# Kernel optimization log

Hardware: AMD Instinct MI355X
Metric: run time of the kernel (lower is better)

## Reference

```python
import jax, jax.numpy as jnp
import numpy as np

E, T, D, DFF = 8, 16384, 512, 2048  # experts, tokens, d_model, d_ff
ROUTE_P = 0.25  # ~ top_k=2 of E=8


def setup_inputs() -> dict:
    key = jax.random.key(0)
    k_x, k_m, k_w1, k_w2 = jax.random.split(key, 4)
    x = jax.random.normal(k_x, (T, D), dtype=jnp.float32)
    mask = jax.random.bernoulli(k_m, ROUTE_P, (E, T))  # bool [E, T]
    W1 = jax.random.normal(k_w1, (E, D, DFF), dtype=jnp.float32) * (1.0 / np.sqrt(D).astype(np.float32))
    b1 = jnp.zeros((E, DFF), dtype=jnp.float32)
    W2 = jax.random.normal(k_w2, (E, DFF, D), dtype=jnp.float32) * (1.0 / np.sqrt(DFF).astype(np.float32))
    b2 = jnp.zeros((E, D), dtype=jnp.float32)
    return {"x": x, "W1": W1, "b1": b1, "W2": W2, "b2": b2, "mask": mask}


def reference(x, W1, b1, W2, b2, mask):
    # vmapped per-expert FFN on shared tokens; mask zeroes non-routed tokens.
    # h: [E, T, DFF]
    h = jax.nn.gelu(jnp.einsum('td,edf->etf', x, W1) + b1[:, None, :])
    # y: [E, T, D]
    y = jnp.einsum('etf,efd->etd', h, W2) + b2[:, None, :]
    return jnp.where(mask[:, :, None], y, jnp.zeros((), dtype=y.dtype))
```

## Files before the change

### kernel.cpp

```cpp
#include <hip/hip_runtime.h>
#include <hip/hip_bf16.h>

#define NE 8
#define TOK 16384
#define ND 512
#define NF 2048
#define HP 4608
#define MT 36

typedef __attribute__((ext_vector_type(8))) short bf16x8;
typedef __attribute__((ext_vector_type(4))) float f32x4;
typedef unsigned short u16;
typedef unsigned long long u64;

__device__ __forceinline__ u16 f2bf(float f) {
  union { float f; unsigned u; } c; c.f = f;
  unsigned u = c.u;
  return (u16)((u + 0x7FFFu + ((u >> 16) & 1u)) >> 16);
}

__device__ __forceinline__ float gelu_fast(float x) {
  float x2 = x * x;
  float zp = x * __builtin_fmaf(0.10294325f, x2, 2.3022084f);
  float u = __builtin_amdgcn_exp2f(zp);
  float r = __builtin_amdgcn_rcpf(u + 1.0f);
  return x * (1.0f - r);
}

__device__ __forceinline__ void gl_lds16(const void* g, void* l) {
  __builtin_amdgcn_global_load_lds(
      (const __attribute__((address_space(1))) unsigned int*)g,
      (__attribute__((address_space(3))) unsigned int*)l, 16, 0, 0);
}

__device__ __forceinline__ int swzr(int row) { return ((row >> 1) & 3) << 4; }

__global__ void transpose_bf16(const float* __restrict__ in, u16* __restrict__ out,
                               int R, int C) {
  __shared__ float tile[32][33];
  int e = blockIdx.z;
  const float* ip = in + (size_t)e * R * C;
  u16* op = out + (size_t)e * R * C;
  int c0 = blockIdx.x * 32, r0 = blockIdx.y * 32;
  int tx = threadIdx.x & 31, ty = threadIdx.x >> 5;
  for (int i = 0; i < 32; i += 8)
    tile[ty + i][tx] = ip[(size_t)(r0 + ty + i) * C + (c0 + tx)];
  __syncthreads();
  for (int i = 0; i < 32; i += 8)
    op[(size_t)(c0 + ty + i) * R + (r0 + tx)] = f2bf(tile[tx][ty + i]);
}

__global__ void x_to_bf16(const float* __restrict__ x, u16* __restrict__ xbf) {
  int i = blockIdx.x * 256 + threadIdx.x;
  float4 v = ((const float4*)x)[i];
  union { u16 s[4]; u64 ll; } o;
  o.s[0] = f2bf(v.x); o.s[1] = f2bf(v.y); o.s[2] = f2bf(v.z); o.s[3] = f2bf(v.w);
  ((u64*)xbf)[i] = o.ll;
}

__global__ void zero_unmasked(const int* __restrict__ mask, float4* __restrict__ out4) {
  int row = blockIdx.x * 2 + (threadIdx.x >> 7);
  if (mask[row]) return;
  out4[(size_t)row * 128 + (threadIdx.x & 127)] = float4{0.f, 0.f, 0.f, 0.f};
}

__global__ void compact_mask(const int* __restrict__ mask, int* __restrict__ idx,
                             int* __restrict__ counts) {
  int e = blockIdx.x;
  __shared__ int wsum[4];
  __shared__ int base;
  if (threadIdx.x == 0) base = 0;
  const int* m = mask + (size_t)e * TOK;
  int lane = threadIdx.x & 63, w = threadIdx.x >> 6;
  for (int c0 = 0; c0 < TOK; c0 += 256) {
    __syncthreads();
    int i = c0 + threadIdx.x;
    int mi = (m[i] != 0);
    unsigned long long b = __ballot(mi);
    if (lane == 0) wsum[w] = __popcll(b);
    __syncthreads();
    int off = base;
    for (int ww = 0; ww < w; ww++) off += wsum[ww];
    off += __popcll(b & ((1ull << lane) - 1ull));
    if (mi) idx[(size_t)e * TOK + off] = i;
    __syncthreads();
    if (threadIdx.x == 0) base += wsum[0] + wsum[1] + wsum[2] + wsum[3];
  }
  __syncthreads();
  if (threadIdx.x == 0) counts[e] = base;
}

__launch_bounds__(256, 4)
__global__ void gemm1(const u16* __restrict__ xbf, const u16* __restrict__ W1t,
                      const float* __restrict__ b1f, const int* __restrict__ idx,
                      const int* __restrict__ counts, u16* __restrict__ h) {
  const int BPE = (NF / 128) * MT;
  int bid = blockIdx.x;
  int e = bid / BPE, r = bid % BPE;
  int f0 = (r / MT) * 128, t0 = (r % MT) * 128;
  int cnt = counts[e];
  if (t0 >= cnt) return;

  __shared__ __align__(16) u16 As[2][4096];
  __shared__ __align__(16) u16 Bs[2][4096];

  int tid = threadIdx.x, lane = tid & 63, w = tid >> 6;
  int wm = w & 1, wn = w >> 1;
  int l15 = lane & 15, l4 = lane >> 4;
  const int* idxe = idx + (size_t)e * TOK;

  int srow = lane >> 2, scolb = (lane & 3) << 4;
  int ar0 = w * 16 + srow, ar1 = 64 + w * 16 + srow;
  int cm1 = cnt - 1;
  int tk0 = idxe[t0 + ar0 <= cm1 ? t0 + ar0 : cm1];
  int tk1 = idxe[t0 + ar1 <= cm1 ? t0 + ar1 : cm1];
  const char* xb = (const char*)xbf;
  const char* w1 = (const char*)W1t;
  size_t asrc0 = ((size_t)e * NF + f0 + ar0) * 1024 + (scolb ^ swzr(ar0));
  size_t asrc1 = ((size_t)e * NF + f0 + ar1) * 1024 + (scolb ^ swzr(ar1));
  size_t bsrc0 = (size_t)tk0 * 1024 + (scolb ^ swzr(ar0));
  size_t bsrc1 = (size_t)tk1 * 1024 + (scolb ^ swzr(ar1));

  int aoff[4], boff[4];
  #pragma unroll
  for (int i = 0; i < 4; i++) {
    int rowa = wm * 64 + i * 16 + l15;
    aoff[i] = rowa * 64 + ((l4 * 16) ^ swzr(rowa));
    int rowb = wn * 64 + i * 16 + l15;
    boff[i] = rowb * 64 + ((l4 * 16) ^ swzr(rowb));
  }

  auto STAGE = [&](int kb, int c) {
    char* ad = (char*)As + c * 8192 + w * 1024 + lane * 16;
    char* bd = (char*)Bs + c * 8192 + w * 1024 + lane * 16;
    gl_lds16(w1 + asrc0 + kb * 64, ad);
    gl_lds16(w1 + asrc1 + kb * 64, ad + 4096);
    gl_lds16(xb + bsrc0 + kb * 64, bd);
    gl_lds16(xb + bsrc1 + kb * 64, bd + 4096);
  };

  f32x4 acc[4][4];
  #pragma unroll
  for (int i = 0; i < 4; i++)
    #pragma unroll
    for (int j = 0; j < 4; j++) acc[i][j] = (f32x4)(0.0f);

  STAGE(0, 0);
  __syncthreads();
  #pragma unroll
  for (int kb = 0; kb < 16; ++kb) {
    int cur = kb & 1;
    if (kb < 15) STAGE(kb + 1, cur ^ 1);
    const char* ab = (const char*)As + cur * 8192;
    const char* bb = (const char*)Bs + cur * 8192;
    bf16x8 a[4], b[4];
    #pragma unroll
    for (int i = 0; i < 4; i++) a[i] = *(const bf16x8*)(ab + aoff[i]);
    #pragma unroll
    for (int j = 0; j < 4; j++) b[j] = *(const bf16x8*)(bb + boff[j]);
    #pragma unroll
    for (int i = 0; i < 4; i++)
      #pragma unroll
      for (int j = 0; j < 4; j++)
        acc[i][j] = __builtin_amdgcn_mfma_f32_16x16x32_bf16(a[i], b[j], acc[i][j], 0, 0, 0);
    __syncthreads();
  }

  #pragma unroll
  for (int i = 0; i < 4; i++) {
    int fb = f0 + wm * 64 + i * 16 + l4 * 4;
    f32x4 bv = *(const f32x4*)(b1f + (size_t)e * NF + fb);
    #pragma unroll
    for (int j = 0; j < 4; j++) {
      int t = t0 + wn * 64 + j * 16 + l15;
      union { u16 s[4]; u64 ll; } pk;
      #pragma unroll
      for (int jj = 0; jj < 4; jj++)
        pk.s[jj] = f2bf(gelu_fast(acc[i][j][jj] + bv[jj]));
      *(u64*)(h + ((size_t)e * HP + t) * NF + fb) = pk.ll;
    }
  }
}

__launch_bounds__(256, 4)
__global__ void gemm2(const u16* __restrict__ h, const u16* __restrict__ W2t,
                      const float* __restrict__ b2f, const int* __restrict__ idx,
                      const int* __restrict__ counts, float* __restrict__ out) {
  const int BPE = (ND / 128) * MT;
  int bid = blockIdx.x;
  int e = bid / BPE, r = bid % BPE;
  int d0 = (r / MT) * 128, t0 = (r % MT) * 128;
  int cnt = counts[e];
  if (t0 >= cnt) return;

  __shared__ __align__(16) u16 As[2][4096];
  __shared__ __align__(16) u16 Bs[2][4096];

  int tid = threadIdx.x, lane = tid & 63, w = tid >> 6;
  int wm = w & 1, wn = w >> 1;
  int l15 = lane & 15, l4 = lane >> 4;
  const int* idxe = idx + (size_t)e * TOK;

  int srow = lane >> 2, scolb = (lane & 3) << 4;
  int ar0 = w * 16 + srow, ar1 = 64 + w * 16 + srow;
  const char* hb = (const char*)h;
  const char* w2 = (const char*)W2t;
  size_t asrc0 = ((size_t)e * ND + d0 + ar0) * 4096 + (scolb ^ swzr(ar0));
  size_t asrc1 = ((size_t)e * ND + d0 + ar1) * 4096 + (scolb ^ swzr(ar1));
  size_t bsrc0 = ((size_t)e * HP + t0 + ar0) * 4096 + (scolb ^ swzr(ar0));
  size_t bsrc1 = ((size_t)e * HP + t0 + ar1) * 4096 + (scolb ^ swzr(ar1));

  int aoff[4], boff[4];
  #pragma unroll
  for (int i = 0; i < 4; i++) {
    int rowa = wm * 64 + i * 16 + l15;
    aoff[i] = rowa * 64 + ((l4 * 16) ^ swzr(rowa));
    int rowb = wn * 64 + i * 16 + l15;
    boff[i] = rowb * 64 + ((l4 * 16) ^ swzr(rowb));
  }

  auto STAGE = [&](int kb, int c) {
    char* ad = (char*)As + c * 8192 + w * 1024 + lane * 16;
    char* bd = (char*)Bs + c * 8192 + w * 1024 + lane * 16;
    gl_lds16(w2 + asrc0 + kb * 64, ad);
    gl_lds16(w2 + asrc1 + kb * 64, ad + 4096);
    gl_lds16(hb + bsrc0 + kb * 64, bd);
    gl_lds16(hb + bsrc1 + kb * 64, bd + 4096);
  };

  f32x4 acc[4][4];
  #pragma unroll
  for (int i = 0; i < 4; i++)
    #pragma unroll
    for (int j = 0; j < 4; j++) acc[i][j] = (f32x4)(0.0f);

  STAGE(0, 0);
  __syncthreads();
  #pragma unroll 2
  for (int kb = 0; kb < 64; ++kb) {
    int cur = kb & 1;
    if (kb < 63) STAGE(kb + 1, cur ^ 1);
    const char* ab = (const char*)As + cur * 8192;
    const char* bb = (const char*)Bs + cur * 8192;
    bf16x8 a[4], b[4];
    #pragma unroll
    for (int i = 0; i < 4; i++) a[i] = *(const bf16x8*)(ab + aoff[i]);
    #pragma unroll
    for (int j = 0; j < 4; j++) b[j] = *(const bf16x8*)(bb + boff[j]);
    #pragma unroll
    for (int i = 0; i < 4; i++)
      #pragma unroll
      for (int j = 0; j < 4; j++)
        acc[i][j] = __builtin_amdgcn_mfma_f32_16x16x32_bf16(a[i], b[j], acc[i][j], 0, 0, 0);
    __syncthreads();
  }

  #pragma unroll
  for (int i = 0; i < 4; i++) {
    int db = d0 + wm * 64 + i * 16 + l4 * 4;
    f32x4 b2v = *(const f32x4*)(b2f + (size_t)e * ND + db);
    #pragma unroll
    for (int j = 0; j < 4; j++) {
      int t = t0 + wn * 64 + j * 16 + l15;
      if (t < cnt) {
        int tok = idxe[t];
        f32x4 v;
        #pragma unroll
        for (int jj = 0; jj < 4; jj++) v[jj] = acc[i][j][jj] + b2v[jj];
        *(f32x4*)(out + ((size_t)e * TOK + tok) * ND + db) = v;
      }
    }
  }
}

extern "C" void kernel_launch(void* const* d_in, const int* in_sizes, int n_in,
                              void* d_out, int out_size, void* d_ws, size_t ws_size,
                              hipStream_t stream) {
  const float* x  = (const float*)d_in[0];
  const float* W1 = (const float*)d_in[1];
  const float* b1 = (const float*)d_in[2];
  const float* W2 = (const float*)d_in[3];
  const float* b2 = (const float*)d_in[4];
  const int* mask = (const int*)d_in[5];

  char* ws = (char*)d_ws;
  int* counts = (int*)ws;
  int* idx    = (int*)(ws + 1024);
  u16* W1t    = (u16*)(ws + 1024 + (size_t)NE * TOK * 4);
  u16* W2t    = W1t + (size_t)NE * NF * ND;
  u16* xbf    = W2t + (size_t)NE * ND * NF;
  u16* h      = xbf + (size_t)TOK * ND;

  zero_unmasked<<<dim3(NE * TOK / 2), dim3(256), 0, stream>>>(mask, (float4*)d_out);
  transpose_bf16<<<dim3(NF / 32, ND / 32, NE), dim3(256), 0, stream>>>(W1, W1t, ND, NF);
  transpose_bf16<<<dim3(ND / 32, NF / 32, NE), dim3(256), 0, stream>>>(W2, W2t, NF, ND);
  x_to_bf16<<<dim3(TOK * ND / 4 / 256), dim3(256), 0, stream>>>(x, xbf);
  compact_mask<<<dim3(NE), dim3(256), 0, stream>>>(mask, idx, counts);

  gemm1<<<dim3(NE * (NF / 128) * MT), dim3(256), 0, stream>>>(xbf, W1t, b1, idx, counts, h);
  gemm2<<<dim3(NE * (ND / 128) * MT), dim3(256), 0, stream>>>(h, W2t, b2, idx, counts,
                                                              (float*)d_out);
}
```

Measured before the change: 382.4 us.

## Triple-buffer LDS staging with vmcnt waits and a single barrier per k-step

Both GEMM kernels move from double-buffered to triple-buffered LDS tiles. Loads are issued two k-steps ahead, and explicit s_waitcnt vmcnt waits replace the trailing __syncthreads, so each iteration has one barrier. The aim is to hide global-to-LDS load latency behind MFMA work. In exchange, LDS use per block rises from 32KB to 48KB and launch bounds drop to 3 blocks per CU, which lowers occupancy.

Result: no change. 385.8 us (+0.9%).

```diff
diff --git a/kernel.cpp b/kernel.cpp
--- a/kernel.cpp
+++ b/kernel.cpp
@@ -12,6 +12,8 @@
 typedef __attribute__((ext_vector_type(4))) float f32x4;
 typedef unsigned short u16;
 typedef unsigned long long u64;
+
+#define WAITV(n) asm volatile("s_waitcnt vmcnt(" #n ")" ::: "memory")
 
 __device__ __forceinline__ u16 f2bf(float f) {
   union { float f; unsigned u; } c; c.f = f;
@@ -90,7 +92,7 @@
   if (threadIdx.x == 0) counts[e] = base;
 }
 
-__launch_bounds__(256, 4)
+__launch_bounds__(256, 3)
 __global__ void gemm1(const u16* __restrict__ xbf, const u16* __restrict__ W1t,
                       const float* __restrict__ b1f, const int* __restrict__ idx,
                       const int* __restrict__ counts, u16* __restrict__ h) {
@@ -101,8 +103,8 @@
   int cnt = counts[e];
   if (t0 >= cnt) return;
 
-  __shared__ __align__(16) u16 As[2][4096];
-  __shared__ __align__(16) u16 Bs[2][4096];
+  __shared__ __align__(16) u16 As[3][4096];
+  __shared__ __align__(16) u16 Bs[3][4096];
 
   int tid = threadIdx.x, lane = tid & 63, w = tid >> 6;
   int wm = w & 1, wn = w >> 1;
@@ -130,9 +132,9 @@
     boff[i] = rowb * 64 + ((l4 * 16) ^ swzr(rowb));
   }
 
-  auto STAGE = [&](int kb, int c) {
-    char* ad = (char*)As + c * 8192 + w * 1024 + lane * 16;
-    char* bd = (char*)Bs + c * 8192 + w * 1024 + lane * 16;
+  auto STAGE = [&](int kb, int s) {
+    char* ad = (char*)As + s * 8192 + w * 1024 + lane * 16;
+    char* bd = (char*)Bs + s * 8192 + w * 1024 + lane * 16;
     gl_lds16(w1 + asrc0 + kb * 64, ad);
     gl_lds16(w1 + asrc1 + kb * 64, ad + 4096);
     gl_lds16(xb + bsrc0 + kb * 64, bd);
@@ -146,13 +148,17 @@
     for (int j = 0; j < 4; j++) acc[i][j] = (f32x4)(0.0f);
 
   STAGE(0, 0);
-  __syncthreads();
+  STAGE(1, 1);
+
   #pragma unroll
   for (int kb = 0; kb < 16; ++kb) {
-    int cur = kb & 1;
-    if (kb < 15) STAGE(kb + 1, cur ^ 1);
-    const char* ab = (const char*)As + cur * 8192;
-    const char* bb = (const char*)Bs + cur * 8192;
+    int s = kb % 3;
+    if (kb < 15) WAITV(4);
+    else         WAITV(0);
+    __builtin_amdgcn_s_barrier();
+    if (kb < 14) STAGE(kb + 2, (kb + 2) % 3);
+    const char* ab = (const char*)As + s * 8192;
+    const char* bb = (const char*)Bs + s * 8192;
     bf16x8 a[4], b[4];
     #pragma unroll
     for (int i = 0; i < 4; i++) a[i] = *(const bf16x8*)(ab + aoff[i]);
@@ -163,7 +169,6 @@
       #pragma unroll
       for (int j = 0; j < 4; j++)
         acc[i][j] = __builtin_amdgcn_mfma_f32_16x16x32_bf16(a[i], b[j], acc[i][j], 0, 0, 0);
-    __syncthreads();
   }
 
   #pragma unroll
@@ -182,7 +187,7 @@
   }
 }
 
-__launch_bounds__(256, 4)
+__launch_bounds__(256, 3)
 __global__ void gemm2(const u16* __restrict__ h, const u16* __restrict__ W2t,
                       const float* __restrict__ b2f, const int* __restrict__ idx,
                       const int* __restrict__ counts, float* __restrict__ out) {
@@ -193,8 +198,8 @@
   int cnt = counts[e];
   if (t0 >= cnt) return;
 
-  __shared__ __align__(16) u16 As[2][4096];
-  __shared__ __align__(16) u16 Bs[2][4096];
+  __shared__ __align__(16) u16 As[3][4096];
+  __shared__ __align__(16) u16 Bs[3][4096];
 
   int tid = threadIdx.x, lane = tid & 63, w = tid >> 6;
   int wm = w & 1, wn = w >> 1;
@@ -219,9 +224,9 @@
     boff[i] = rowb * 64 + ((l4 * 16) ^ swzr(rowb));
   }
 
-  auto STAGE = [&](int kb, int c) {
-    char* ad = (char*)As + c * 8192 + w * 1024 + lane * 16;
-    char* bd = (char*)Bs + c * 8192 + w * 1024 + lane * 16;
+  auto STAGE = [&](int kb, int s) {
+    char* ad = (char*)As + s * 8192 + w * 1024 + lane * 16;
+    char* bd = (char*)Bs + s * 8192 + w * 1024 + lane * 16;
     gl_lds16(w2 + asrc0 + kb * 64, ad);
     gl_lds16(w2 + asrc1 + kb * 64, ad + 4096);
     gl_lds16(hb + bsrc0 + kb * 64, bd);
@@ -235,13 +240,16 @@
     for (int j = 0; j < 4; j++) acc[i][j] = (f32x4)(0.0f);
 
   STAGE(0, 0);
-  __syncthreads();
-  #pragma unroll 2
-  for (int kb = 0; kb < 64; ++kb) {
-    int cur = kb & 1;
-    if (kb < 63) STAGE(kb + 1, cur ^ 1);
-    const char* ab = (const char*)As + cur * 8192;
-    const char* bb = (const char*)Bs + cur * 8192;
+  STAGE(1, 1);
+
+  int s0 = 0, s1 = 1, s2 = 2;
+  #pragma unroll 3
+  for (int kb = 0; kb < 63; ++kb) {
+    WAITV(4);
+    __builtin_amdgcn_s_barrier();
+    if (kb < 62) STAGE(kb + 2, s2);
+    const char* ab = (const char*)As + s0 * 8192;
+    const char* bb = (const char*)Bs + s0 * 8192;
     bf16x8 a[4], b[4];
     #pragma unroll
     for (int i = 0; i < 4; i++) a[i] = *(const bf16x8*)(ab + aoff[i]);
@@ -252,7 +260,23 @@
       #pragma unroll
       for (int j = 0; j < 4; j++)
         acc[i][j] = __builtin_amdgcn_mfma_f32_16x16x32_bf16(a[i], b[j], acc[i][j], 0, 0, 0);
-    __syncthreads();
+    int tt = s0; s0 = s1; s1 = s2; s2 = tt;
+  }
+  {
+    WAITV(0);
+    __builtin_amdgcn_s_barrier();
+    const char* ab = (const char*)As + s0 * 8192;
+    const char* bb = (const char*)Bs + s0 * 8192;
+    bf16x8 a[4], b[4];
+    #pragma unroll
+    for (int i = 0; i < 4; i++) a[i] = *(const bf16x8*)(ab + aoff[i]);
+    #pragma unroll
+    for (int j = 0; j < 4; j++) b[j] = *(const bf16x8*)(bb + boff[j]);
+    #pragma unroll
+    for (int i = 0; i < 4; i++)
+      #pragma unroll
+      for (int j = 0; j < 4; j++)
+        acc[i][j] = __builtin_amdgcn_mfma_f32_16x16x32_bf16(a[i], b[j], acc[i][j], 0, 0, 0);
   }
 
   #pragma unroll
```

## Restructure MoE GEMMs into 512-thread 128x256 tiles with triple-buffered interleaved pipeline

Applied to the files above, without the earlier changes.

Both expert GEMMs move to 512-thread blocks, each computing a 128x256 output tile with a K step of 64. Staging uses three LDS buffers, so loads run two K-tiles ahead, and a new XOR swizzle matches the wider rows. The K-tile is split into four MFMA phases interleaved with LDS fragment loads and staged global loads, with explicit vmcnt/lgkmcnt waits, barriers and s_setprio around MFMA bursts. This is meant to hide global and LDS latency and raise data reuse per block. In exchange it uses more LDS and registers, which lowers occupancy, and adds more barriers per K-tile.

Result: no change. 380.8 us (-0.4%).

```diff
diff --git a/kernel.cpp b/kernel.cpp
--- a/kernel.cpp
+++ b/kernel.cpp
@@ -6,12 +6,16 @@
 #define ND 512
 #define NF 2048
 #define HP 4608
-#define MT 36
 
 typedef __attribute__((ext_vector_type(8))) short bf16x8;
 typedef __attribute__((ext_vector_type(4))) float f32x4;
 typedef unsigned short u16;
 typedef unsigned long long u64;
+
+#define WAITV(n) asm volatile("s_waitcnt vmcnt(" #n ")" ::: "memory")
+#define LGKM0()  asm volatile("s_waitcnt lgkmcnt(0)" ::: "memory")
+#define SBAR()   __builtin_amdgcn_s_barrier()
+#define PRIO(p)  __builtin_amdgcn_s_setprio(p)
 
 __device__ __forceinline__ u16 f2bf(float f) {
   union { float f; unsigned u; } c; c.f = f;
@@ -32,8 +36,6 @@
       (const __attribute__((address_space(1))) unsigned int*)g,
       (__attribute__((address_space(3))) unsigned int*)l, 16, 0, 0);
 }
-
-__device__ __forceinline__ int swzr(int row) { return ((row >> 1) & 3) << 4; }
 
 __global__ void transpose_bf16(const float* __restrict__ in, u16* __restrict__ out,
                                int R, int C) {
@@ -90,54 +92,73 @@
   if (threadIdx.x == 0) counts[e] = base;
 }
 
-__launch_bounds__(256, 4)
+
+__launch_bounds__(512, 2)
 __global__ void gemm1(const u16* __restrict__ xbf, const u16* __restrict__ W1t,
                       const float* __restrict__ b1f, const int* __restrict__ idx,
                       const int* __restrict__ counts, u16* __restrict__ h) {
-  const int BPE = (NF / 128) * MT;
   int bid = blockIdx.x;
-  int e = bid / BPE, r = bid % BPE;
-  int f0 = (r / MT) * 128, t0 = (r % MT) * 128;
+  int e = bid / 288, r = bid % 288;
+  int f0 = (r / 18) * 128, t0 = (r % 18) * 256;
   int cnt = counts[e];
   if (t0 >= cnt) return;
 
-  __shared__ __align__(16) u16 As[2][4096];
-  __shared__ __align__(16) u16 Bs[2][4096];
+  __shared__ __align__(16) u16 lds[3 * 24576];
 
   int tid = threadIdx.x, lane = tid & 63, w = tid >> 6;
   int wm = w & 1, wn = w >> 1;
   int l15 = lane & 15, l4 = lane >> 4;
   const int* idxe = idx + (size_t)e * TOK;
-
-  int srow = lane >> 2, scolb = (lane & 3) << 4;
-  int ar0 = w * 16 + srow, ar1 = 64 + w * 16 + srow;
   int cm1 = cnt - 1;
-  int tk0 = idxe[t0 + ar0 <= cm1 ? t0 + ar0 : cm1];
-  int tk1 = idxe[t0 + ar1 <= cm1 ? t0 + ar1 : cm1];
+
+  int srow = w * 16 + (lane >> 3);
+  int ssw = ((lane & 7) * 16) ^ ((srow & 7) << 4);
+  const char* w1 = (const char*)W1t;
   const char* xb = (const char*)xbf;
-  const char* w1 = (const char*)W1t;
-  size_t asrc0 = ((size_t)e * NF + f0 + ar0) * 1024 + (scolb ^ swzr(ar0));
-  size_t asrc1 = ((size_t)e * NF + f0 + ar1) * 1024 + (scolb ^ swzr(ar1));
-  size_t bsrc0 = (size_t)tk0 * 1024 + (scolb ^ swzr(ar0));
-  size_t bsrc1 = (size_t)tk1 * 1024 + (scolb ^ swzr(ar1));
-
-  int aoff[4], boff[4];
+  size_t aS = ((size_t)e * NF + f0 + srow) * 1024 + ssw;
+  int tA0 = idxe[(t0 + srow)       <= cm1 ? (t0 + srow)       : cm1];
+  int tA1 = idxe[(t0 + srow + 8)   <= cm1 ? (t0 + srow + 8)   : cm1];
+  int tB0 = idxe[(t0 + srow + 128) <= cm1 ? (t0 + srow + 128) : cm1];
+  int tB1 = idxe[(t0 + srow + 136) <= cm1 ? (t0 + srow + 136) : cm1];
+  size_t xS0 = (size_t)tA0 * 1024 + ssw, xS1 = (size_t)tA1 * 1024 + ssw;
+  size_t xS2 = (size_t)tB0 * 1024 + ssw, xS3 = (size_t)tB1 * 1024 + ssw;
+
+  int aoff[4][2], boff[4][2];
   #pragma unroll
   for (int i = 0; i < 4; i++) {
-    int rowa = wm * 64 + i * 16 + l15;
-    aoff[i] = rowa * 64 + ((l4 * 16) ^ swzr(rowa));
-    int rowb = wn * 64 + i * 16 + l15;
-    boff[i] = rowb * 64 + ((l4 * 16) ^ swzr(rowb));
-  }
-
-  auto STAGE = [&](int kb, int c) {
-    char* ad = (char*)As + c * 8192 + w * 1024 + lane * 16;
-    char* bd = (char*)Bs + c * 8192 + w * 1024 + lane * 16;
-    gl_lds16(w1 + asrc0 + kb * 64, ad);
-    gl_lds16(w1 + asrc1 + kb * 64, ad + 4096);
-    gl_lds16(xb + bsrc0 + kb * 64, bd);
-    gl_lds16(xb + bsrc1 + kb * 64, bd + 4096);
-  };
+    int ra = wm * 64 + i * 16 + l15;
+    int rb = wn * 64 + i * 16 + l15;
+    #pragma unroll
+    for (int ks = 0; ks < 2; ks++) {
+      aoff[i][ks] = ra * 128 + ((ks * 64 + l4 * 16) ^ ((ra & 7) << 4));
+      boff[i][ks] = 16384 + rb * 128 + ((ks * 64 + l4 * 16) ^ ((rb & 7) << 4));
+    }
+  }
+
+  auto SA = [&](int kt, char* bp) {
+    char* d = bp + w * 2048;
+    gl_lds16(w1 + aS + kt * 128, d);
+    gl_lds16(w1 + aS + 8192 + kt * 128, d + 1024);
+  };
+  auto SB0 = [&](int kt, char* bp) {
+    char* d = bp + 16384 + w * 2048;
+    gl_lds16(xb + xS0 + kt * 128, d);
+    gl_lds16(xb + xS1 + kt * 128, d + 1024);
+  };
+  auto SB1 = [&](int kt, char* bp) {
+    char* d = bp + 32768 + w * 2048;
+    gl_lds16(xb + xS2 + kt * 128, d);
+    gl_lds16(xb + xS3 + kt * 128, d + 1024);
+  };
+
+  char* bc = (char*)lds;
+  char* bn = (char*)lds + 49152;
+  char* bs = (char*)lds + 98304;
+
+  SA(0, bc); SB0(0, bc); SB1(0, bc);
+  SA(1, bn); SB0(1, bn); SB1(1, bn);
+  WAITV(6);
+  SBAR();
 
   f32x4 acc[4][4];
   #pragma unroll
@@ -145,25 +166,67 @@
     #pragma unroll
     for (int j = 0; j < 4; j++) acc[i][j] = (f32x4)(0.0f);
 
-  STAGE(0, 0);
-  __syncthreads();
-  #pragma unroll
-  for (int kb = 0; kb < 16; ++kb) {
-    int cur = kb & 1;
-    if (kb < 15) STAGE(kb + 1, cur ^ 1);
-    const char* ab = (const char*)As + cur * 8192;
-    const char* bb = (const char*)Bs + cur * 8192;
-    bf16x8 a[4], b[4];
-    #pragma unroll
-    for (int i = 0; i < 4; i++) a[i] = *(const bf16x8*)(ab + aoff[i]);
-    #pragma unroll
-    for (int j = 0; j < 4; j++) b[j] = *(const bf16x8*)(bb + boff[j]);
-    #pragma unroll
-    for (int i = 0; i < 4; i++)
+  bf16x8 A0[4], A1[4], Ba[2], Bb[2];
+  #pragma unroll
+  for (int i = 0; i < 4; i++) A0[i] = *(const bf16x8*)(bc + aoff[i][0]);
+  Ba[0] = *(const bf16x8*)(bc + boff[0][0]);
+  Ba[1] = *(const bf16x8*)(bc + boff[1][0]);
+
+  const int nt = 8;
+  for (int t = 0; t < nt; ++t) {
+    bool stg = (t + 2 < nt);
+    if (stg) SA(t + 2, bs);
+    Bb[0] = *(const bf16x8*)(bc + boff[2][0]);
+    Bb[1] = *(const bf16x8*)(bc + boff[3][0]);
+    PRIO(1);
+    #pragma unroll
+    for (int i = 0; i < 4; i++) {
+      acc[i][0] = __builtin_amdgcn_mfma_f32_16x16x32_bf16(A0[i], Ba[0], acc[i][0], 0, 0, 0);
+      acc[i][1] = __builtin_amdgcn_mfma_f32_16x16x32_bf16(A0[i], Ba[1], acc[i][1], 0, 0, 0);
+    }
+    PRIO(0);
+    LGKM0(); SBAR();
+    if (stg) SB0(t + 2, bs);
+    #pragma unroll
+    for (int i = 0; i < 4; i++) A1[i] = *(const bf16x8*)(bc + aoff[i][1]);
+    Ba[0] = *(const bf16x8*)(bc + boff[0][1]);
+    Ba[1] = *(const bf16x8*)(bc + boff[1][1]);
+    PRIO(1);
+    #pragma unroll
+    for (int i = 0; i < 4; i++) {
+      acc[i][2] = __builtin_amdgcn_mfma_f32_16x16x32_bf16(A0[i], Bb[0], acc[i][2], 0, 0, 0);
+      acc[i][3] = __builtin_amdgcn_mfma_f32_16x16x32_bf16(A0[i], Bb[1], acc[i][3], 0, 0, 0);
+    }
+    PRIO(0);
+    LGKM0(); SBAR();
+    if (stg) SB1(t + 2, bs);
+    Bb[0] = *(const bf16x8*)(bc + boff[2][1]);
+    Bb[1] = *(const bf16x8*)(bc + boff[3][1]);
+    PRIO(1);
+    #pragma unroll
+    for (int i = 0; i < 4; i++) {
+      acc[i][0] = __builtin_amdgcn_mfma_f32_16x16x32_bf16(A1[i], Ba[0], acc[i][0], 0, 0, 0);
+      acc[i][1] = __builtin_amdgcn_mfma_f32_16x16x32_bf16(A1[i], Ba[1], acc[i][1], 0, 0, 0);
+    }
+    PRIO(0);
+    if (stg) WAITV(6);
+    else     WAITV(0);
+    LGKM0(); SBAR();
+    if (t + 1 < nt) {
       #pragma unroll
-      for (int j = 0; j < 4; j++)
-        acc[i][j] = __builtin_amdgcn_mfma_f32_16x16x32_bf16(a[i], b[j], acc[i][j], 0, 0, 0);
-    __syncthreads();
+      for (int i = 0; i < 4; i++) A0[i] = *(const bf16x8*)(bn + aoff[i][0]);
+      Ba[0] = *(const bf16x8*)(bn + boff[0][0]);
+      Ba[1] = *(const bf16x8*)(bn + boff[1][0]);
+    }
+    PRIO(1);
+    #pragma unroll
+    for (int i = 0; i < 4; i++) {
+      acc[i][2] = __builtin_amdgcn_mfma_f32_16x16x32_bf16(A1[i], Bb[0], acc[i][2], 0, 0, 0);
+      acc[i][3] = __builtin_amdgcn_mfma_f32_16x16x32_bf16(A1[i], Bb[1], acc[i][3], 0, 0, 0);
+    }
+    PRIO(0);
+    LGKM0(); SBAR();
+    char* tp = bc; bc = bn; bn = bs; bs = tp;
   }
 
   #pragma unroll
@@ -182,51 +245,66 @@
   }
 }
 
-__launch_bounds__(256, 4)
+__launch_bounds__(512, 2)
 __global__ void gemm2(const u16* __restrict__ h, const u16* __restrict__ W2t,
                       const float* __restrict__ b2f, const int* __restrict__ idx,
                       const int* __restrict__ counts, float* __restrict__ out) {
-  const int BPE = (ND / 128) * MT;
   int bid = blockIdx.x;
-  int e = bid / BPE, r = bid % BPE;
-  int d0 = (r / MT) * 128, t0 = (r % MT) * 128;
+  int e = bid / 72, r = bid % 72;
+  int d0 = (r / 18) * 128, t0 = (r % 18) * 256;
   int cnt = counts[e];
   if (t0 >= cnt) return;
 
-  __shared__ __align__(16) u16 As[2][4096];
-  __shared__ __align__(16) u16 Bs[2][4096];
+  __shared__ __align__(16) u16 lds[3 * 24576];
 
   int tid = threadIdx.x, lane = tid & 63, w = tid >> 6;
   int wm = w & 1, wn = w >> 1;
   int l15 = lane & 15, l4 = lane >> 4;
   const int* idxe = idx + (size_t)e * TOK;
 
-  int srow = lane >> 2, scolb = (lane & 3) << 4;
-  int ar0 = w * 16 + srow, ar1 = 64 + w * 16 + srow;
+  int srow = w * 16 + (lane >> 3);
+  int ssw = ((lane & 7) * 16) ^ ((srow & 7) << 4);
+  const char* w2 = (const char*)W2t;
   const char* hb = (const char*)h;
-  const char* w2 = (const char*)W2t;
-  size_t asrc0 = ((size_t)e * ND + d0 + ar0) * 4096 + (scolb ^ swzr(ar0));
-  size_t asrc1 = ((size_t)e * ND + d0 + ar1) * 4096 + (scolb ^ swzr(ar1));
-  size_t bsrc0 = ((size_t)e * HP + t0 + ar0) * 4096 + (scolb ^ swzr(ar0));
-  size_t bsrc1 = ((size_t)e * HP + t0 + ar1) * 4096 + (scolb ^ swzr(ar1));
-
-  int aoff[4], boff[4];
+  size_t aS = ((size_t)e * ND + d0 + srow) * 4096 + ssw;
+  size_t bS = ((size_t)e * HP + t0 + srow) * 4096 + ssw;
+
+  int aoff[4][2], boff[4][2];
   #pragma unroll
   for (int i = 0; i < 4; i++) {
-    int rowa = wm * 64 + i * 16 + l15;
-    aoff[i] = rowa * 64 + ((l4 * 16) ^ swzr(rowa));
-    int rowb = wn * 64 + i * 16 + l15;
-    boff[i] = rowb * 64 + ((l4 * 16) ^ swzr(rowb));
-  }
-
-  auto STAGE = [&](int kb, int c) {
-    char* ad = (char*)As + c * 8192 + w * 1024 + lane * 16;
-    char* bd = (char*)Bs + c * 8192 + w * 1024 + lane * 16;
-    gl_lds16(w2 + asrc0 + kb * 64, ad);
-    gl_lds16(w2 + asrc1 + kb * 64, ad + 4096);
-    gl_lds16(hb + bsrc0 + kb * 64, bd);
-    gl_lds16(hb + bsrc1 + kb * 64, bd + 4096);
-  };
+    int ra = wm * 64 + i * 16 + l15;
+    int rb = wn * 64 + i * 16 + l15;
+    #pragma unroll
+    for (int ks = 0; ks < 2; ks++) {
+      aoff[i][ks] = ra * 128 + ((ks * 64 + l4 * 16) ^ ((ra & 7) << 4));
+      boff[i][ks] = 16384 + rb * 128 + ((ks * 64 + l4 * 16) ^ ((rb & 7) << 4));
+    }
+  }
+
+  auto SA = [&](int kt, char* bp) {
+    char* d = bp + w * 2048;
+    gl_lds16(w2 + aS + kt * 128, d);
+    gl_lds16(w2 + aS + 8 * 4096 + kt * 128, d + 1024);
+  };
+  auto SB0 = [&](int kt, char* bp) {
+    char* d = bp + 16384 + w * 2048;
+    gl_lds16(hb + bS + kt * 128, d);
+    gl_lds16(hb + bS + 8 * 4096 + kt * 128, d + 1024);
+  };
+  auto SB1 = [&](int kt, char* bp) {
+    char* d = bp + 32768 + w * 2048;
+    gl_lds16(hb + bS + 128 * 4096 + kt * 128, d);
+    gl_lds16(hb + bS + 136 * 4096 + kt * 128, d + 1024);
+  };
+
+  char* bc = (char*)lds;
+  char* bn = (char*)lds + 49152;
+  char* bs = (char*)lds + 98304;
+
+  SA(0, bc); SB0(0, bc); SB1(0, bc);
+  SA(1, bn); SB0(1, bn); SB1(1, bn);
+  WAITV(6);
+  SBAR();
 
   f32x4 acc[4][4];
   #pragma unroll
@@ -234,25 +312,67 @@
     #pragma unroll
     for (int j = 0; j < 4; j++) acc[i][j] = (f32x4)(0.0f);
 
-  STAGE(0, 0);
-  __syncthreads();
-  #pragma unroll 2
-  for (int kb = 0; kb < 64; ++kb) {
-    int cur = kb & 1;
-    if (kb < 63) STAGE(kb + 1, cur ^ 1);
-    const char* ab = (const char*)As + cur * 8192;
-    const char* bb = (const char*)Bs + cur * 8192;
-    bf16x8 a[4], b[4];
-    #pragma unroll
-    for (int i = 0; i < 4; i++) a[i] = *(const bf16x8*)(ab + aoff[i]);
-    #pragma unroll
-    for (int j = 0; j < 4; j++) b[j] = *(const bf16x8*)(bb + boff[j]);
-    #pragma unroll
-    for (int i = 0; i < 4; i++)
+  bf16x8 A0[4], A1[4], Ba[2], Bb[2];
+  #pragma unroll
+  for (int i = 0; i < 4; i++) A0[i] = *(const bf16x8*)(bc + aoff[i][0]);
+  Ba[0] = *(const bf16x8*)(bc + boff[0][0]);
+  Ba[1] = *(const bf16x8*)(bc + boff[1][0]);
+
+  const int nt = 32;
+  for (int t = 0; t < nt; ++t) {
+    bool stg = (t + 2 < nt);
+    if (stg) SA(t + 2, bs);
+    Bb[0] = *(const bf16x8*)(bc + boff[2][0]);
+    Bb[1] = *(const bf16x8*)(bc + boff[3][0]);
+    PRIO(1);
+    #pragma unroll
+    for (int i = 0; i < 4; i++) {
+      acc[i][0] = __builtin_amdgcn_mfma_f32_16x16x32_bf16(A0[i], Ba[0], acc[i][0], 0, 0, 0);
+      acc[i][1] = __builtin_amdgcn_mfma_f32_16x16x32_bf16(A0[i], Ba[1], acc[i][1], 0, 0, 0);
+    }
+    PRIO(0);
+    LGKM0(); SBAR();
+    if (stg) SB0(t + 2, bs);
+    #pragma unroll
+    for (int i = 0; i < 4; i++) A1[i] = *(const bf16x8*)(bc + aoff[i][1]);
+    Ba[0] = *(const bf16x8*)(bc + boff[0][1]);
+    Ba[1] = *(const bf16x8*)(bc + boff[1][1]);
+    PRIO(1);
+    #pragma unroll
+    for (int i = 0; i < 4; i++) {
+      acc[i][2] = __builtin_amdgcn_mfma_f32_16x16x32_bf16(A0[i], Bb[0], acc[i][2], 0, 0, 0);
+      acc[i][3] = __builtin_amdgcn_mfma_f32_16x16x32_bf16(A0[i], Bb[1], acc[i][3], 0, 0, 0);
+    }
+    PRIO(0);
+    LGKM0(); SBAR();
+    if (stg) SB1(t + 2, bs);
+    Bb[0] = *(const bf16x8*)(bc + boff[2][1]);
+    Bb[1] = *(const bf16x8*)(bc + boff[3][1]);
+    PRIO(1);
+    #pragma unroll
+    for (int i = 0; i < 4; i++) {
+      acc[i][0] = __builtin_amdgcn_mfma_f32_16x16x32_bf16(A1[i], Ba[0], acc[i][0], 0, 0, 0);
+      acc[i][1] = __builtin_amdgcn_mfma_f32_16x16x32_bf16(A1[i], Ba[1], acc[i][1], 0, 0, 0);
+    }
+    PRIO(0);
+    if (stg) WAITV(6);
+    else     WAITV(0);
+    LGKM0(); SBAR();
+    if (t + 1 < nt) {
       #pragma unroll
-      for (int j = 0; j < 4; j++)
-        acc[i][j] = __builtin_amdgcn_mfma_f32_16x16x32_bf16(a[i], b[j], acc[i][j], 0, 0, 0);
-    __syncthreads();
+      for (int i = 0; i < 4; i++) A0[i] = *(const bf16x8*)(bn + aoff[i][0]);
+      Ba[0] = *(const bf16x8*)(bn + boff[0][0]);
+      Ba[1] = *(const bf16x8*)(bn + boff[1][0]);
+    }
+    PRIO(1);
+    #pragma unroll
+    for (int i = 0; i < 4; i++) {
+      acc[i][2] = __builtin_amdgcn_mfma_f32_16x16x32_bf16(A1[i], Bb[0], acc[i][2], 0, 0, 0);
+      acc[i][3] = __builtin_amdgcn_mfma_f32_16x16x32_bf16(A1[i], Bb[1], acc[i][3], 0, 0, 0);
+    }
+    PRIO(0);
+    LGKM0(); SBAR();
+    char* tp = bc; bc = bn; bn = bs; bs = tp;
   }
 
   #pragma unroll
@@ -297,7 +417,7 @@
   x_to_bf16<<<dim3(TOK * ND / 4 / 256), dim3(256), 0, stream>>>(x, xbf);
   compact_mask<<<dim3(NE), dim3(256), 0, stream>>>(mask, idx, counts);
 
-  gemm1<<<dim3(NE * (NF / 128) * MT), dim3(256), 0, stream>>>(xbf, W1t, b1, idx, counts, h);
-  gemm2<<<dim3(NE * (ND / 128) * MT), dim3(256), 0, stream>>>(h, W2t, b2, idx, counts,
-                                                              (float*)d_out);
-}
+  gemm1<<<dim3(NE * 16 * 18), dim3(512), 0, stream>>>(xbf, W1t, b1, idx, counts, h);
+  gemm2<<<dim3(NE * 4 * 18), dim3(512), 0, stream>>>(h, W2t, b2, idx, counts,
+                                                     (float*)d_out);
+}
```

## Gather routed tokens into per-expert compact bf16 buffer before gemm1

Applied to the files above, without the earlier changes.

Replaces the dense x-to-bf16 conversion with a gather kernel that writes each expert's routed tokens contiguously in bf16, so gemm1 reads its B operand with plain strided addressing instead of per-row indirect token lookups. The compact_mask kernel is also widened to 1024 threads per block to cut its serial iteration count. This trades a larger per-expert activation buffer (padded to HP rows per expert) and duplicated token reads for more contiguous, cache-friendly loads in gemm1.

Result: faster. 374.9 us (-2.0%).

```diff
diff --git a/kernel.cpp b/kernel.cpp
--- a/kernel.cpp
+++ b/kernel.cpp
@@ -50,14 +50,6 @@
     op[(size_t)(c0 + ty + i) * R + (r0 + tx)] = f2bf(tile[tx][ty + i]);
 }
 
-__global__ void x_to_bf16(const float* __restrict__ x, u16* __restrict__ xbf) {
-  int i = blockIdx.x * 256 + threadIdx.x;
-  float4 v = ((const float4*)x)[i];
-  union { u16 s[4]; u64 ll; } o;
-  o.s[0] = f2bf(v.x); o.s[1] = f2bf(v.y); o.s[2] = f2bf(v.z); o.s[3] = f2bf(v.w);
-  ((u64*)xbf)[i] = o.ll;
-}
-
 __global__ void zero_unmasked(const int* __restrict__ mask, float4* __restrict__ out4) {
   int row = blockIdx.x * 2 + (threadIdx.x >> 7);
   if (mask[row]) return;
@@ -67,12 +59,12 @@
 __global__ void compact_mask(const int* __restrict__ mask, int* __restrict__ idx,
                              int* __restrict__ counts) {
   int e = blockIdx.x;
-  __shared__ int wsum[4];
+  __shared__ int wsum[16];
   __shared__ int base;
   if (threadIdx.x == 0) base = 0;
   const int* m = mask + (size_t)e * TOK;
   int lane = threadIdx.x & 63, w = threadIdx.x >> 6;
-  for (int c0 = 0; c0 < TOK; c0 += 256) {
+  for (int c0 = 0; c0 < TOK; c0 += 1024) {
     __syncthreads();
     int i = c0 + threadIdx.x;
     int mi = (m[i] != 0);
@@ -84,15 +76,34 @@
     off += __popcll(b & ((1ull << lane) - 1ull));
     if (mi) idx[(size_t)e * TOK + off] = i;
     __syncthreads();
-    if (threadIdx.x == 0) base += wsum[0] + wsum[1] + wsum[2] + wsum[3];
+    if (threadIdx.x == 0) {
+      int s = 0;
+      #pragma unroll
+      for (int k = 0; k < 16; k++) s += wsum[k];
+      base += s;
+    }
   }
   __syncthreads();
   if (threadIdx.x == 0) counts[e] = base;
 }
 
+__global__ void gather_xc(const float* __restrict__ x, const int* __restrict__ idx,
+                          const int* __restrict__ counts, u16* __restrict__ xc) {
+  int e = blockIdx.y;
+  int r = blockIdx.x * 2 + (threadIdx.x >> 7);
+  int cnt = counts[e];
+  int rr = r < cnt ? r : cnt - 1;
+  int tok = idx[(size_t)e * TOK + rr];
+  int c4 = (threadIdx.x & 127) << 2;
+  float4 v = *(const float4*)(x + (size_t)tok * ND + c4);
+  union { u16 s[4]; u64 ll; } o;
+  o.s[0] = f2bf(v.x); o.s[1] = f2bf(v.y); o.s[2] = f2bf(v.z); o.s[3] = f2bf(v.w);
+  *(u64*)(xc + ((size_t)e * HP + r) * ND + c4) = o.ll;
+}
+
 __launch_bounds__(256, 4)
-__global__ void gemm1(const u16* __restrict__ xbf, const u16* __restrict__ W1t,
-                      const float* __restrict__ b1f, const int* __restrict__ idx,
+__global__ void gemm1(const u16* __restrict__ xc, const u16* __restrict__ W1t,
+                      const float* __restrict__ b1f,
                       const int* __restrict__ counts, u16* __restrict__ h) {
   const int BPE = (NF / 128) * MT;
   int bid = blockIdx.x;
@@ -107,19 +118,15 @@
   int tid = threadIdx.x, lane = tid & 63, w = tid >> 6;
   int wm = w & 1, wn = w >> 1;
   int l15 = lane & 15, l4 = lane >> 4;
-  const int* idxe = idx + (size_t)e * TOK;
 
   int srow = lane >> 2, scolb = (lane & 3) << 4;
   int ar0 = w * 16 + srow, ar1 = 64 + w * 16 + srow;
-  int cm1 = cnt - 1;
-  int tk0 = idxe[t0 + ar0 <= cm1 ? t0 + ar0 : cm1];
-  int tk1 = idxe[t0 + ar1 <= cm1 ? t0 + ar1 : cm1];
-  const char* xb = (const char*)xbf;
+  const char* xb = (const char*)xc;
   const char* w1 = (const char*)W1t;
   size_t asrc0 = ((size_t)e * NF + f0 + ar0) * 1024 + (scolb ^ swzr(ar0));
   size_t asrc1 = ((size_t)e * NF + f0 + ar1) * 1024 + (scolb ^ swzr(ar1));
-  size_t bsrc0 = (size_t)tk0 * 1024 + (scolb ^ swzr(ar0));
-  size_t bsrc1 = (size_t)tk1 * 1024 + (scolb ^ swzr(ar1));
+  size_t bsrc0 = ((size_t)e * HP + t0 + ar0) * 1024 + (scolb ^ swzr(ar0));
+  size_t bsrc1 = ((size_t)e * HP + t0 + ar1) * 1024 + (scolb ^ swzr(ar1));
 
   int aoff[4], boff[4];
   #pragma unroll
@@ -288,16 +295,16 @@
   int* idx    = (int*)(ws + 1024);
   u16* W1t    = (u16*)(ws + 1024 + (size_t)NE * TOK * 4);
   u16* W2t    = W1t + (size_t)NE * NF * ND;
-  u16* xbf    = W2t + (size_t)NE * ND * NF;
-  u16* h      = xbf + (size_t)TOK * ND;
+  u16* xc     = W2t + (size_t)NE * ND * NF;
+  u16* h      = xc + (size_t)NE * HP * ND;
 
   zero_unmasked<<<dim3(NE * TOK / 2), dim3(256), 0, stream>>>(mask, (float4*)d_out);
   transpose_bf16<<<dim3(NF / 32, ND / 32, NE), dim3(256), 0, stream>>>(W1, W1t, ND, NF);
   transpose_bf16<<<dim3(ND / 32, NF / 32, NE), dim3(256), 0, stream>>>(W2, W2t, NF, ND);
-  x_to_bf16<<<dim3(TOK * ND / 4 / 256), dim3(256), 0, stream>>>(x, xbf);
-  compact_mask<<<dim3(NE), dim3(256), 0, stream>>>(mask, idx, counts);
-
-  gemm1<<<dim3(NE * (NF / 128) * MT), dim3(256), 0, stream>>>(xbf, W1t, b1, idx, counts, h);
+  compact_mask<<<dim3(NE), dim3(1024), 0, stream>>>(mask, idx, counts);
+  gather_xc<<<dim3(HP / 2, NE), dim3(256), 0, stream>>>(x, idx, counts, xc);
+
+  gemm1<<<dim3(NE * (NF / 128) * MT), dim3(256), 0, stream>>>(xc, W1t, b1, counts, h);
   gemm2<<<dim3(NE * (ND / 128) * MT), dim3(256), 0, stream>>>(h, W2t, b2, idx, counts,
                                                               (float*)d_out);
 }
```
